# Performance work log

Hardware: AMD Instinct MI355X
Metric: run time of the kernel (lower is better)

The kernel has to match this reference:

```python
import jax, jax.numpy as jnp
import numpy as np
from jax import lax


def _conv(x, w, padding, groups=1):
    # NCHW / OIHW 2D conv, stride 1
    return lax.conv_general_dilated(
        x, w, window_strides=(1, 1), padding=padding,
        dimension_numbers=("NCHW", "OIHW", "NCHW"),
        feature_group_count=groups)


def setup_inputs() -> dict:
    key = jax.random.key(0)
    ks = jax.random.split(key, 5)
    B, C, H, W = 8, 192, 128, 128
    HEADS = 8
    rgb = jax.random.normal(ks[0], (B, C, H, W), dtype=jnp.float32)
    ir = jax.random.normal(ks[1], (B, C, H, W), dtype=jnp.float32)
    w_qkv = jax.random.normal(ks[2], (3 * C, C, 1, 1), dtype=jnp.float32) * 0.02
    w_dw = jax.random.normal(ks[3], (3 * C, 1, 3, 3), dtype=jnp.float32) * 0.02
    w_proj = jax.random.normal(ks[4], (C, C, 1, 1), dtype=jnp.float32) * 0.02
    temperature = jnp.ones((HEADS, 1, 1), dtype=jnp.float32)
    return {"rgb": rgb, "ir": ir, "w_qkv": w_qkv, "w_dw": w_dw,
            "w_proj": w_proj, "temperature": temperature}


def reference(rgb, ir, w_qkv, w_dw, w_proj, temperature):
    heads = temperature.shape[0]
    b, c, h, w = rgb.shape
    hd = c // heads  # per-head channel count

    def qkv(x):
        y = _conv(x, w_qkv, "VALID")                 # [b, 3c, h, w]
        y = _conv(y, w_dw, "SAME", groups=3 * c)      # depthwise 3x3
        q, k, v = jnp.split(y, 3, axis=1)
        rs = lambda t: t.reshape(b, heads, hd, h * w)  # b head c (h w)
        return rs(q), rs(k), rs(v)

    rq, rk, rv = qkv(rgb)
    iq, ik, iv = qkv(ir)

    # torch F.normalize(dim=-1): x / max(||x||_2, 1e-12)
    nrm = lambda t: t / jnp.maximum(jnp.linalg.norm(t, axis=-1, keepdims=True), 1e-12)
    rq, rk, iq, ik = nrm(rq), nrm(rk), nrm(iq), nrm(ik)

    # channel-wise (transposed) cross attention: [b,h,hd,hd] attn matrices
    attn_ir = jax.nn.softmax(jnp.einsum("bhcn,bhdn->bhcd", rq, ik) * temperature, axis=-1)
    attn_rgb = jax.nn.softmax(jnp.einsum("bhcn,bhdn->bhcd", iq, rk) * temperature, axis=-1)

    out_ir = jnp.einsum("bhcd,bhdn->bhcn", attn_ir, iv).reshape(b, c, h, w)
    out_rgb = jnp.einsum("bhcd,bhdn->bhcn", attn_rgb, rv).reshape(b, c, h, w)

    out_ir = _conv(out_ir, w_proj, "VALID")
    out_rgb = _conv(out_rgb, w_proj, "VALID")
    return out_rgb, out_ir
```

## Files before the change

kernel.cpp:

```cpp
#include <hip/hip_runtime.h>

#define N_PIX 16384
#define CC    192
#define C3    576
#define KK    192
#define HD    24
#define KS    64

typedef __attribute__((ext_vector_type(8))) short short8;
typedef __attribute__((ext_vector_type(4))) float f32x4;

__device__ __forceinline__ unsigned short f2bf(float x) {
    unsigned u = __float_as_uint(x);
    u += 0x7fff + ((u >> 16) & 1);
    return (unsigned short)(u >> 16);
}
__device__ __forceinline__ float bf2f(unsigned short s) {
    return __uint_as_float(((unsigned)s) << 16);
}
__device__ __forceinline__ int pack2(unsigned short lo, unsigned short hi) {
    return (int)(((unsigned)hi << 16) | (unsigned)lo);
}

__device__ __forceinline__ void g2l16(const unsigned short* g, unsigned short* l) {
    __builtin_amdgcn_global_load_lds(
        (const __attribute__((address_space(1))) void*)g,
        (__attribute__((address_space(3))) void*)l, 16, 0, 0);
}

__global__ __launch_bounds__(256) void cvt_f32_bf16(const float* __restrict__ src,
                                                    unsigned short* __restrict__ dst, int n4) {
    int i = blockIdx.x * 256 + threadIdx.x;
    if (i < n4) {
        float4 v = ((const float4*)src)[i];
        ushort4 o;
        o.x = f2bf(v.x); o.y = f2bf(v.y); o.z = f2bf(v.z); o.w = f2bf(v.w);
        ((ushort4*)dst)[i] = o;
    }
}

__global__ __launch_bounds__(256) void cvtT(const float* __restrict__ rgb,
                                            const float* __restrict__ ir,
                                            unsigned short* __restrict__ xT) {
    const int z  = blockIdx.y;
    const int n0 = blockIdx.x * 128;
    const float* x = ((z >= 8) ? ir : rgb) + (long)(z & 7) * CC * N_PIX;
    __shared__ unsigned short T[192][136];

    const int t = threadIdx.x;
#pragma unroll
    for (int i = 0; i < 24; i++) {
        int q = i * 256 + t;
        int k = q >> 5, nc = q & 31;
        float4 v = *(const float4*)(x + (long)k * N_PIX + n0 + nc * 4);
        ushort4 o;
        o.x = f2bf(v.x); o.y = f2bf(v.y); o.z = f2bf(v.z); o.w = f2bf(v.w);
        *(ushort4*)&T[k][nc * 4] = o;
    }
    __syncthreads();
    unsigned short* dst = xT + ((long)z * N_PIX + n0) * CC;
#pragma unroll
    for (int i = 0; i < 12; i++) {
        int c = i * 256 + t;
        int n = c / 24, kc = c - n * 24;
        unsigned short us[8];
#pragma unroll
        for (int j = 0; j < 8; j++) us[j] = T[kc * 8 + j][n];
        int4 pk = make_int4(pack2(us[0], us[1]), pack2(us[2], us[3]),
                            pack2(us[4], us[5]), pack2(us[6], us[7]));
        *(int4*)(dst + (long)n * CC + kc * 8) = pk;
    }
}

__global__ __launch_bounds__(512, 4) void qkv_mfma(const unsigned short* __restrict__ wbf,
                                                   const unsigned short* __restrict__ xT,
                                                   unsigned short* __restrict__ Ybf) {
    const int z  = blockIdx.z;
    const unsigned short* Bg = xT + (long)z * N_PIX * CC;
    unsigned short* y = Ybf + (long)z * C3 * N_PIX;
    const int m0 = blockIdx.y * 192, n0 = blockIdx.x * 128;

    __shared__ unsigned short As[2][192 * 64];
    __shared__ unsigned short Bs[2][128 * 64];

    const int tid  = threadIdx.x;
    const int wave = tid >> 6, lane = tid & 63;
    const int quad = lane >> 4, l15 = lane & 15;
    const int wr = wave >> 2, wc = wave & 3;

    f32x4 acc[6][2];
#pragma unroll
    for (int i = 0; i < 6; i++)
#pragma unroll
        for (int j = 0; j < 2; j++) acc[i][j] = (f32x4)0.f;

    auto stage = [&](int buf, int k0) {
#pragma unroll
        for (int s = 0; s < 3; s++) {
            int j = s * 8 + wave;
            int q = j * 64 + lane;
            int m = q >> 3, c = (q & 7) ^ (m & 7);
            g2l16(wbf + (long)(m0 + m) * KK + k0 + c * 8, &As[buf][j * 512]);
        }
#pragma unroll
        for (int s = 0; s < 2; s++) {
            int j = s * 8 + wave;
            int q = j * 64 + lane;
            int n = q >> 3, c = (q & 7) ^ (n & 7);
            g2l16(Bg + (long)(n0 + n) * CC + k0 + c * 8, &Bs[buf][j * 512]);
        }
    };

    stage(0, 0);
    __syncthreads();
    int cur = 0;
    for (int it = 0; it < 3; ++it) {
        if (it < 2) stage(cur ^ 1, (it + 1) * KS);
        const unsigned short* A  = As[cur];
        const unsigned short* Bl = Bs[cur];
#pragma unroll
        for (int kk = 0; kk < 2; kk++) {
            short8 a[6], b[2];
#pragma unroll
            for (int mi = 0; mi < 6; mi++) {
                int r = wr * 96 + mi * 16 + l15;
                int c = (kk * 4 + quad) ^ (r & 7);
                a[mi] = *(const short8*)&A[r * 64 + c * 8];
            }
#pragma unroll
            for (int ni = 0; ni < 2; ni++) {
                int n = wc * 32 + ni * 16 + l15;
                int c = (kk * 4 + quad) ^ (n & 7);
                b[ni] = *(const short8*)&Bl[n * 64 + c * 8];
            }
#pragma unroll
            for (int mi = 0; mi < 6; mi++)
#pragma unroll
                for (int ni = 0; ni < 2; ni++)
                    acc[mi][ni] = __builtin_amdgcn_mfma_f32_16x16x32_bf16(a[mi], b[ni], acc[mi][ni], 0, 0, 0);
        }
        __syncthreads();
        cur ^= 1;
    }

#pragma unroll
    for (int mi = 0; mi < 6; mi++)
#pragma unroll
        for (int ni = 0; ni < 2; ni++)
#pragma unroll
            for (int r = 0; r < 4; r++) {
                int row = m0 + wr * 96 + mi * 16 + quad * 4 + r;
                int col = n0 + wc * 32 + ni * 16 + l15;
                y[(long)row * N_PIX + col] = f2bf(acc[mi][ni][r]);
            }
}

__device__ __forceinline__ void mfma_gemm_old(const unsigned short* __restrict__ Abf,
                                              const unsigned short* __restrict__ Bsrc,
                                              float* __restrict__ Cdst,
                                              int m0, int n0) {
    __shared__ unsigned short As[192][44];
    __shared__ unsigned short Bs[128][44];

    const int tid  = threadIdx.x;
    const int wave = tid >> 6, lane = tid & 63;
    const int quad = lane >> 4, l15 = lane & 15;
    const int wr = wave >> 2, wc = wave & 3;

    f32x4 acc[6][2];
#pragma unroll
    for (int i = 0; i < 6; i++)
#pragma unroll
        for (int j = 0; j < 2; j++) acc[i][j] = (f32x4)0.f;

    const int kg = tid & 7;
    const int n2 = tid >> 3;

    for (int k0 = 0; k0 < KK; k0 += 32) {
        {
            int row = tid >> 2, kc = (tid & 3) * 8;
            *(int4*)&As[row][kc] = *(const int4*)(Abf + (long)(m0 + row) * KK + k0 + kc);
            if (tid < 256) {
                int ch = tid + 512;
                int row2 = ch >> 2, kc2 = (ch & 3) * 8;
                *(int4*)&As[row2][kc2] = *(const int4*)(Abf + (long)(m0 + row2) * KK + k0 + kc2);
            }
        }
        {
            ushort2 v[4];
#pragma unroll
            for (int j = 0; j < 4; j++)
                v[j] = *(const ushort2*)(Bsrc + (long)(k0 + kg * 4 + j) * N_PIX + n0 + n2 * 2);
#pragma unroll
            for (int i = 0; i < 2; i++) {
                unsigned short us[4];
#pragma unroll
                for (int j = 0; j < 4; j++) us[j] = i ? v[j].y : v[j].x;
                int2 pk = make_int2(pack2(us[0], us[1]), pack2(us[2], us[3]));
                *(int2*)&Bs[n2 * 2 + i][kg * 4] = pk;
            }
        }
        __syncthreads();

        short8 a[6], b[2];
#pragma unroll
        for (int mi = 0; mi < 6; mi++)
            a[mi] = *(const short8*)&As[wr * 96 + mi * 16 + l15][quad * 8];
#pragma unroll
        for (int ni = 0; ni < 2; ni++)
            b[ni] = *(const short8*)&Bs[wc * 32 + ni * 16 + l15][quad * 8];
#pragma unroll
        for (int mi = 0; mi < 6; mi++)
#pragma unroll
            for (int ni = 0; ni < 2; ni++)
                acc[mi][ni] = __builtin_amdgcn_mfma_f32_16x16x32_bf16(a[mi], b[ni], acc[mi][ni], 0, 0, 0);
        __syncthreads();
    }

#pragma unroll
    for (int mi = 0; mi < 6; mi++)
#pragma unroll
        for (int ni = 0; ni < 2; ni++)
#pragma unroll
            for (int r = 0; r < 4; r++) {
                int row = m0 + wr * 96 + mi * 16 + quad * 4 + r;
                int col = n0 + wc * 32 + ni * 16 + l15;
                Cdst[(long)row * N_PIX + col] = acc[mi][ni][r];
            }
}

__global__ __launch_bounds__(512, 4) void out_mfma(const unsigned short* __restrict__ weff,
                                                   const unsigned short* __restrict__ Zbf,
                                                   float* __restrict__ out) {
    const int z = blockIdx.z;
    const unsigned short* V = Zbf + ((long)z * C3 + 2 * CC) * N_PIX;
    float* C = out + (long)z * CC * N_PIX;
    mfma_gemm_old(weff + (long)z * CC * CC, V, C, 0, blockIdx.x * 128);
}

__global__ __launch_bounds__(256) void dwconv3x3(const unsigned short* __restrict__ Ybf,
                                                 const float* __restrict__ wdw,
                                                 unsigned short* __restrict__ Zbf) {
    const int z  = blockIdx.z;
    const int oc = blockIdx.y;
    const int idx = blockIdx.x * 256 + threadIdx.x;
    const int p0  = idx * 8;
    const int h   = p0 >> 7;
    const int w0  = p0 & 127;
    const int wq  = threadIdx.x & 15;
    const unsigned short* Yc = Ybf + ((long)z * C3 + oc) * N_PIX;

    float wk[9];
#pragma unroll
    for (int i = 0; i < 9; i++) wk[i] = wdw[oc * 9 + i];

    float f[3][8];
#pragma unroll
    for (int ry = 0; ry < 3; ry++) {
        const int hy = h + ry - 1;
        int4 raw = make_int4(0, 0, 0, 0);
        if (hy >= 0 && hy <= 127)
            raw = *(const int4*)(Yc + hy * 128 + w0);
        f[ry][0] = bf2f((unsigned short)(raw.x & 0xffff));
        f[ry][1] = bf2f((unsigned short)((unsigned)raw.x >> 16));
        f[ry][2] = bf2f((unsigned short)(raw.y & 0xffff));
        f[ry][3] = bf2f((unsigned short)((unsigned)raw.y >> 16));
        f[ry][4] = bf2f((unsigned short)(raw.z & 0xffff));
        f[ry][5] = bf2f((unsigned short)((unsigned)raw.z >> 16));
        f[ry][6] = bf2f((unsigned short)(raw.w & 0xffff));
        f[ry][7] = bf2f((unsigned short)((unsigned)raw.w >> 16));
    }

    float acc[8];
#pragma unroll
    for (int j = 0; j < 8; j++) acc[j] = 0.f;

#pragma unroll
    for (int ry = 0; ry < 3; ry++) {
        float l = __shfl_up(f[ry][7], 1);
        float r = __shfl_down(f[ry][0], 1);
        if (wq == 0)  l = 0.f;
        if (wq == 15) r = 0.f;
        const float wl = wk[ry * 3 + 0], wc = wk[ry * 3 + 1], wr = wk[ry * 3 + 2];
        acc[0] = fmaf(wl, l, acc[0]);
#pragma unroll
        for (int j = 1; j < 8; j++) acc[j] = fmaf(wl, f[ry][j - 1], acc[j]);
#pragma unroll
        for (int j = 0; j < 8; j++) acc[j] = fmaf(wc, f[ry][j], acc[j]);
#pragma unroll
        for (int j = 0; j < 7; j++) acc[j] = fmaf(wr, f[ry][j + 1], acc[j]);
        acc[7] = fmaf(wr, r, acc[7]);
    }

    ushort4 o[2];
    unsigned short* po = (unsigned short*)o;
#pragma unroll
    for (int j = 0; j < 8; j++) po[j] = f2bf(acc[j]);
    *(int4*)(Zbf + ((long)z * C3 + oc) * N_PIX + p0) = *(const int4*)o;
}

__global__ __launch_bounds__(64) void gram_partial(const unsigned short* __restrict__ Zbf,
                                                   float* __restrict__ gpart) {
    const int split = blockIdx.x;
    const int bh    = blockIdx.y;
    const int which = blockIdx.z;
    const int b = bh >> 3, head = bh & 7;
    const int zq = (which == 0) ? b : 8 + b;
    const int zk = (which == 0) ? 8 + b : b;
    const unsigned short* Q  = Zbf + ((long)zq * C3 + head * HD) * N_PIX;
    const unsigned short* Kr = Zbf + ((long)zk * C3 + CC + head * HD) * N_PIX;

    __shared__ float Qc[24][132];
    __shared__ float Kc[24][132];

    const int t = threadIdx.x;
    const int ci = t >> 3, di = t & 7;
    const int c0 = ci * 3, d0 = di * 3;

    float acc[3][3];
#pragma unroll
    for (int i = 0; i < 3; i++)
#pragma unroll
        for (int j = 0; j < 3; j++) acc[i][j] = 0.f;
    float ss = 0.f;

    const int n0base = split * 2048;
    for (int nc = 0; nc < 2048; nc += 128) {
        const long n0 = n0base + nc;
        const unsigned short* src = nullptr;
        float* dstrow = nullptr;
        if (t < 24)               { src = Q  + (long)t * N_PIX + n0;        dstrow = Qc[t]; }
        else if (t >= 32 && t < 56) { src = Kr + (long)(t - 32) * N_PIX + n0; dstrow = Kc[t - 32]; }
        if (src) {
#pragma unroll 4
            for (int i = 0; i < 16; i++) {
                int4 raw = *(const int4*)(src + i * 8);
                float f[8];
                f[0] = bf2f((unsigned short)(raw.x & 0xffff)); f[1] = bf2f((unsigned short)((unsigned)raw.x >> 16));
                f[2] = bf2f((unsigned short)(raw.y & 0xffff)); f[3] = bf2f((unsigned short)((unsigned)raw.y >> 16));
                f[4] = bf2f((unsigned short)(raw.z & 0xffff)); f[5] = bf2f((unsigned short)((unsigned)raw.z >> 16));
                f[6] = bf2f((unsigned short)(raw.w & 0xffff)); f[7] = bf2f((unsigned short)((unsigned)raw.w >> 16));
                *(float4*)&dstrow[i * 8]     = make_float4(f[0], f[1], f[2], f[3]);
                *(float4*)&dstrow[i * 8 + 4] = make_float4(f[4], f[5], f[6], f[7]);
#pragma unroll
                for (int q = 0; q < 8; q++) ss = fmaf(f[q], f[q], ss);
            }
        }
        __syncthreads();
#pragma unroll 4
        for (int kk = 0; kk < 128; kk += 4) {
            float4 qv[3], kv[3];
#pragma unroll
            for (int i = 0; i < 3; i++) qv[i] = *(const float4*)&Qc[c0 + i][kk];
#pragma unroll
            for (int j = 0; j < 3; j++) kv[j] = *(const float4*)&Kc[d0 + j][kk];
#pragma unroll
            for (int i = 0; i < 3; i++)
#pragma unroll
                for (int j = 0; j < 3; j++)
                    acc[i][j] += qv[i].x * kv[j].x + qv[i].y * kv[j].y +
                                 qv[i].z * kv[j].z + qv[i].w * kv[j].w;
        }
        __syncthreads();
    }

    const int g = (which * 64 + bh) * 8 + split;
    float* gp = gpart + (long)g * 624;
#pragma unroll
    for (int i = 0; i < 3; i++)
#pragma unroll
        for (int j = 0; j < 3; j++)
            gp[(c0 + i) * 24 + (d0 + j)] = acc[i][j];
    if (t < 24) gp[576 + t] = ss;
    else if (t >= 32 && t < 56) gp[600 + (t - 32)] = ss;
}

__global__ __launch_bounds__(256) void gram_reduce_softmax(const float* __restrict__ gpart,
                                                           const float* __restrict__ temperature,
                                                           float* __restrict__ P) {
    const int g = blockIdx.x;
    const int head = g & 7;
    __shared__ float Gs[576];
    __shared__ float qs[24], ks[24], invq[24], invk[24];

    const int t = threadIdx.x;
    for (int e = t; e < 624; e += 256) {
        float s = 0.f;
        for (int sp = 0; sp < 8; sp++) s += gpart[(long)(g * 8 + sp) * 624 + e];
        if (e < 576) Gs[e] = s;
        else if (e < 600) qs[e - 576] = s;
        else ks[e - 600] = s;
    }
    __syncthreads();
    if (t < 24) {
        invq[t] = 1.f / fmaxf(sqrtf(qs[t]), 1e-12f);
        invk[t] = 1.f / fmaxf(sqrtf(ks[t]), 1e-12f);
    }
    __syncthreads();
    if (t < 24) {
        const float temp = temperature[head];
        float row[24];
        float m = -1e30f;
#pragma unroll
        for (int d = 0; d < 24; d++) {
            row[d] = Gs[t * 24 + d] * invq[t] * invk[d] * temp;
            m = fmaxf(m, row[d]);
        }
        float ssum = 0.f;
#pragma unroll
        for (int d = 0; d < 24; d++) {
            row[d] = expf(row[d] - m);
            ssum += row[d];
        }
        const float inv = 1.f / ssum;
#pragma unroll
        for (int d = 0; d < 24; d++)
            P[(long)g * 576 + t * 24 + d] = row[d] * inv;
    }
}

__global__ __launch_bounds__(256) void build_weff(const float* __restrict__ wproj,
                                                  const float* __restrict__ P,
                                                  unsigned short* __restrict__ weff) {
    const int o = blockIdx.z, b = blockIdx.y;
    const int e = blockIdx.x * 256 + threadIdx.x;
    const int co = e / 192, col = e % 192;
    const int head = col / 24, d = col % 24;
    const int which = 1 - o;
    const float* Pp = P + (long)(which * 64 + b * 8 + head) * 576;
    const float* wp = wproj + co * 192 + head * 24;
    float acc = 0.f;
#pragma unroll
    for (int hc = 0; hc < 24; hc++)
        acc = fmaf(wp[hc], Pp[hc * 24 + d], acc);
    weff[((long)(o * 8 + b) * 192 + co) * 192 + col] = f2bf(acc);
}

extern "C" void kernel_launch(void* const* d_in, const int* in_sizes, int n_in,
                              void* d_out, int out_size, void* d_ws, size_t ws_size,
                              hipStream_t stream) {
    (void)in_sizes; (void)n_in; (void)out_size; (void)ws_size;
    const float* rgb    = (const float*)d_in[0];
    const float* ir     = (const float*)d_in[1];
    const float* w_qkv  = (const float*)d_in[2];
    const float* w_dw   = (const float*)d_in[3];
    const float* w_proj = (const float*)d_in[4];
    const float* temp   = (const float*)d_in[5];
    float* out = (float*)d_out;

    char* wsb = (char*)d_ws;
    unsigned short* Y_bf    = (unsigned short*)(wsb);
    unsigned short* Z_bf    = (unsigned short*)(wsb + 301989888L);
    unsigned short* xT_bf   = Z_bf;
    unsigned short* w_bf    = (unsigned short*)(wsb + 603979776L);
    unsigned short* weff_bf = (unsigned short*)(wsb + 604200960L);
    float*          gpart   = (float*)(wsb + 605380608L);
    float*          P       = (float*)(wsb + 607936512L);

    cvt_f32_bf16<<<108, 256, 0, stream>>>(w_qkv, w_bf, 27648);
    cvtT<<<dim3(128, 16), 256, 0, stream>>>(rgb, ir, xT_bf);
    qkv_mfma<<<dim3(128, 3, 16), 512, 0, stream>>>(w_bf, xT_bf, Y_bf);
    dwconv3x3<<<dim3(8, 576, 16), 256, 0, stream>>>(Y_bf, w_dw, Z_bf);
    gram_partial<<<dim3(8, 64, 2), 64, 0, stream>>>(Z_bf, gpart);
    gram_reduce_softmax<<<128, 256, 0, stream>>>(gpart, temp, P);
    build_weff<<<dim3(144, 8, 2), 256, 0, stream>>>(w_proj, P, weff_bf);
    out_mfma<<<dim3(128, 1, 16), 512, 0, stream>>>(weff_bf, Z_bf, out);
}
```

Before: 799.4 us.

## Compute Q·K Gram matrices with MFMA and fuse L2 norms into dwconv

Replaces the scalar fp32 per-head Gram kernel with a bf16 MFMA kernel. Each block computes the full 192x192 Q·K^T product for one batch/direction over a 512-pixel slice and keeps only the diagonal 24x24 head blocks. The squared-norm accumulation moves into the depthwise conv epilogue through wave reductions and atomics, and the softmax kernel now reads those norms and sums 32 split partials. This computes 8x more products than needed (off-diagonal blocks are discarded), adds atomics and a zeroing launch, and reuses the Y buffer region for the partials.

```diff
diff --git a/kernel.cpp b/kernel.cpp
--- a/kernel.cpp
+++ b/kernel.cpp
@@ -5,7 +5,7 @@
 #define C3    576
 #define KK    192
 #define HD    24
-#define KS    64
+#define GSPLIT 32
 
 typedef __attribute__((ext_vector_type(8))) short short8;
 typedef __attribute__((ext_vector_type(4))) float f32x4;
@@ -39,6 +39,11 @@
     }
 }
 
+__global__ __launch_bounds__(256) void zero_f32(float* __restrict__ p, int n) {
+    int i = blockIdx.x * 256 + threadIdx.x;
+    if (i < n) p[i] = 0.f;
+}
+
 __global__ __launch_bounds__(256) void cvtT(const float* __restrict__ rgb,
                                             const float* __restrict__ ir,
                                             unsigned short* __restrict__ xT) {
@@ -115,7 +120,7 @@
     __syncthreads();
     int cur = 0;
     for (int it = 0; it < 3; ++it) {
-        if (it < 2) stage(cur ^ 1, (it + 1) * KS);
+        if (it < 2) stage(cur ^ 1, (it + 1) * 64);
         const unsigned short* A  = As[cur];
         const unsigned short* Bl = Bs[cur];
 #pragma unroll
@@ -152,6 +157,90 @@
                 int row = m0 + wr * 96 + mi * 16 + quad * 4 + r;
                 int col = n0 + wc * 32 + ni * 16 + l15;
                 y[(long)row * N_PIX + col] = f2bf(acc[mi][ni][r]);
+            }
+}
+
+__global__ __launch_bounds__(512, 2) void gram_mfma(const unsigned short* __restrict__ Zbf,
+                                                    float* __restrict__ gpart) {
+    const int ks = blockIdx.x;
+    const int zp = blockIdx.y;
+    const int which = zp >> 3, b = zp & 7;
+    const int zq = which ? 8 + b : b;
+    const int zk = which ? b : 8 + b;
+    const unsigned short* Qg = Zbf + (long)zq * C3 * N_PIX;
+    const unsigned short* Kg = Zbf + ((long)zk * C3 + CC) * N_PIX;
+
+    __shared__ unsigned short Qs[2][192 * 64];
+    __shared__ unsigned short Ks[2][192 * 64];
+
+    const int tid  = threadIdx.x;
+    const int wave = tid >> 6, lane = tid & 63;
+    const int quad = lane >> 4, l15 = lane & 15;
+    const int wr = wave >> 1, wc = wave & 1;
+
+    f32x4 acc[3][6];
+#pragma unroll
+    for (int i = 0; i < 3; i++)
+#pragma unroll
+        for (int j = 0; j < 6; j++) acc[i][j] = (f32x4)0.f;
+
+    const int base = ks * 512;
+
+    auto stage = [&](int buf, int k0) {
+#pragma unroll
+        for (int s = 0; s < 3; s++) {
+            int j = s * 8 + wave;
+            int q = j * 64 + lane;
+            int m = q >> 3, c = (q & 7) ^ (m & 7);
+            g2l16(Qg + (long)m * N_PIX + k0 + c * 8, &Qs[buf][j * 512]);
+            g2l16(Kg + (long)m * N_PIX + k0 + c * 8, &Ks[buf][j * 512]);
+        }
+    };
+
+    stage(0, base);
+    __syncthreads();
+    int cur = 0;
+    for (int it = 0; it < 8; ++it) {
+        if (it < 7) stage(cur ^ 1, base + (it + 1) * 64);
+        const unsigned short* Q = Qs[cur];
+        const unsigned short* Kl = Ks[cur];
+#pragma unroll
+        for (int kk = 0; kk < 2; kk++) {
+            short8 a[3], bf[6];
+#pragma unroll
+            for (int mi = 0; mi < 3; mi++) {
+                int r = wr * 48 + mi * 16 + l15;
+                int c = (kk * 4 + quad) ^ (r & 7);
+                a[mi] = *(const short8*)&Q[r * 64 + c * 8];
+            }
+#pragma unroll
+            for (int ni = 0; ni < 6; ni++) {
+                int n = wc * 96 + ni * 16 + l15;
+                int c = (kk * 4 + quad) ^ (n & 7);
+                bf[ni] = *(const short8*)&Kl[n * 64 + c * 8];
+            }
+#pragma unroll
+            for (int mi = 0; mi < 3; mi++)
+#pragma unroll
+                for (int ni = 0; ni < 6; ni++)
+                    acc[mi][ni] = __builtin_amdgcn_mfma_f32_16x16x32_bf16(a[mi], bf[ni], acc[mi][ni], 0, 0, 0);
+        }
+        __syncthreads();
+        cur ^= 1;
+    }
+
+#pragma unroll
+    for (int mi = 0; mi < 3; mi++)
+#pragma unroll
+        for (int ni = 0; ni < 6; ni++)
+#pragma unroll
+            for (int r = 0; r < 4; r++) {
+                int row = wr * 48 + mi * 16 + quad * 4 + r;
+                int col = wc * 96 + ni * 16 + l15;
+                int hr = row / 24, hc = col / 24;
+                if (hr == hc)
+                    gpart[(((long)zp * GSPLIT + ks) * 8 + hr) * 576 +
+                          (row - hr * 24) * 24 + (col - hc * 24)] = acc[mi][ni][r];
             }
 }
 
@@ -240,7 +329,8 @@
 
 __global__ __launch_bounds__(256) void dwconv3x3(const unsigned short* __restrict__ Ybf,
                                                  const float* __restrict__ wdw,
-                                                 unsigned short* __restrict__ Zbf) {
+                                                 unsigned short* __restrict__ Zbf,
+                                                 float* __restrict__ norm) {
     const int z  = blockIdx.z;
     const int oc = blockIdx.y;
     const int idx = blockIdx.x * 256 + threadIdx.x;
@@ -297,105 +387,45 @@
 #pragma unroll
     for (int j = 0; j < 8; j++) po[j] = f2bf(acc[j]);
     *(int4*)(Zbf + ((long)z * C3 + oc) * N_PIX + p0) = *(const int4*)o;
-}
-
-__global__ __launch_bounds__(64) void gram_partial(const unsigned short* __restrict__ Zbf,
-                                                   float* __restrict__ gpart) {
-    const int split = blockIdx.x;
-    const int bh    = blockIdx.y;
-    const int which = blockIdx.z;
-    const int b = bh >> 3, head = bh & 7;
-    const int zq = (which == 0) ? b : 8 + b;
-    const int zk = (which == 0) ? 8 + b : b;
-    const unsigned short* Q  = Zbf + ((long)zq * C3 + head * HD) * N_PIX;
-    const unsigned short* Kr = Zbf + ((long)zk * C3 + CC + head * HD) * N_PIX;
-
-    __shared__ float Qc[24][132];
-    __shared__ float Kc[24][132];
-
-    const int t = threadIdx.x;
-    const int ci = t >> 3, di = t & 7;
-    const int c0 = ci * 3, d0 = di * 3;
-
-    float acc[3][3];
-#pragma unroll
-    for (int i = 0; i < 3; i++)
-#pragma unroll
-        for (int j = 0; j < 3; j++) acc[i][j] = 0.f;
-    float ss = 0.f;
-
-    const int n0base = split * 2048;
-    for (int nc = 0; nc < 2048; nc += 128) {
-        const long n0 = n0base + nc;
-        const unsigned short* src = nullptr;
-        float* dstrow = nullptr;
-        if (t < 24)               { src = Q  + (long)t * N_PIX + n0;        dstrow = Qc[t]; }
-        else if (t >= 32 && t < 56) { src = Kr + (long)(t - 32) * N_PIX + n0; dstrow = Kc[t - 32]; }
-        if (src) {
-#pragma unroll 4
-            for (int i = 0; i < 16; i++) {
-                int4 raw = *(const int4*)(src + i * 8);
-                float f[8];
-                f[0] = bf2f((unsigned short)(raw.x & 0xffff)); f[1] = bf2f((unsigned short)((unsigned)raw.x >> 16));
-                f[2] = bf2f((unsigned short)(raw.y & 0xffff)); f[3] = bf2f((unsigned short)((unsigned)raw.y >> 16));
-                f[4] = bf2f((unsigned short)(raw.z & 0xffff)); f[5] = bf2f((unsigned short)((unsigned)raw.z >> 16));
-                f[6] = bf2f((unsigned short)(raw.w & 0xffff)); f[7] = bf2f((unsigned short)((unsigned)raw.w >> 16));
-                *(float4*)&dstrow[i * 8]     = make_float4(f[0], f[1], f[2], f[3]);
-                *(float4*)&dstrow[i * 8 + 4] = make_float4(f[4], f[5], f[6], f[7]);
-#pragma unroll
-                for (int q = 0; q < 8; q++) ss = fmaf(f[q], f[q], ss);
-            }
-        }
-        __syncthreads();
-#pragma unroll 4
-        for (int kk = 0; kk < 128; kk += 4) {
-            float4 qv[3], kv[3];
-#pragma unroll
-            for (int i = 0; i < 3; i++) qv[i] = *(const float4*)&Qc[c0 + i][kk];
-#pragma unroll
-            for (int j = 0; j < 3; j++) kv[j] = *(const float4*)&Kc[d0 + j][kk];
-#pragma unroll
-            for (int i = 0; i < 3; i++)
-#pragma unroll
-                for (int j = 0; j < 3; j++)
-                    acc[i][j] += qv[i].x * kv[j].x + qv[i].y * kv[j].y +
-                                 qv[i].z * kv[j].z + qv[i].w * kv[j].w;
-        }
-        __syncthreads();
-    }
-
-    const int g = (which * 64 + bh) * 8 + split;
-    float* gp = gpart + (long)g * 624;
-#pragma unroll
-    for (int i = 0; i < 3; i++)
-#pragma unroll
-        for (int j = 0; j < 3; j++)
-            gp[(c0 + i) * 24 + (d0 + j)] = acc[i][j];
-    if (t < 24) gp[576 + t] = ss;
-    else if (t >= 32 && t < 56) gp[600 + (t - 32)] = ss;
+
+    if (oc < 2 * CC) {
+        float ss = 0.f;
+#pragma unroll
+        for (int j = 0; j < 8; j++) {
+            float v = bf2f(po[j]);
+            ss = fmaf(v, v, ss);
+        }
+#pragma unroll
+        for (int off = 32; off > 0; off >>= 1)
+            ss += __shfl_down(ss, off);
+        if ((threadIdx.x & 63) == 0)
+            atomicAdd(&norm[z * (2 * CC) + oc], ss);
+    }
 }
 
 __global__ __launch_bounds__(256) void gram_reduce_softmax(const float* __restrict__ gpart,
+                                                           const float* __restrict__ norm,
                                                            const float* __restrict__ temperature,
                                                            float* __restrict__ P) {
     const int g = blockIdx.x;
-    const int head = g & 7;
+    const int which = g >> 6, b = (g >> 3) & 7, head = g & 7;
+    const int zp = which * 8 + b;
+    const int zq = which ? 8 + b : b;
+    const int zk = which ? b : 8 + b;
     __shared__ float Gs[576];
-    __shared__ float qs[24], ks[24], invq[24], invk[24];
+    __shared__ float invq[24], invk[24];
 
     const int t = threadIdx.x;
-    for (int e = t; e < 624; e += 256) {
+    for (int e = t; e < 576; e += 256) {
         float s = 0.f;
-        for (int sp = 0; sp < 8; sp++) s += gpart[(long)(g * 8 + sp) * 624 + e];
-        if (e < 576) Gs[e] = s;
-        else if (e < 600) qs[e - 576] = s;
-        else ks[e - 600] = s;
-    }
-    __syncthreads();
-    if (t < 24) {
-        invq[t] = 1.f / fmaxf(sqrtf(qs[t]), 1e-12f);
-        invk[t] = 1.f / fmaxf(sqrtf(ks[t]), 1e-12f);
-    }
+        for (int sp = 0; sp < GSPLIT; sp++)
+            s += gpart[(((long)zp * GSPLIT + sp) * 8 + head) * 576 + e];
+        Gs[e] = s;
+    }
+    if (t < 24)
+        invq[t] = 1.f / fmaxf(sqrtf(norm[zq * (2 * CC) + head * HD + t]), 1e-12f);
+    else if (t >= 32 && t < 56)
+        invk[t - 32] = 1.f / fmaxf(sqrtf(norm[zk * (2 * CC) + CC + head * HD + (t - 32)]), 1e-12f);
     __syncthreads();
     if (t < 24) {
         const float temp = temperature[head];
@@ -452,17 +482,19 @@
     unsigned short* Y_bf    = (unsigned short*)(wsb);
     unsigned short* Z_bf    = (unsigned short*)(wsb + 301989888L);
     unsigned short* xT_bf   = Z_bf;
+    float*          gpart   = (float*)(wsb);
     unsigned short* w_bf    = (unsigned short*)(wsb + 603979776L);
     unsigned short* weff_bf = (unsigned short*)(wsb + 604200960L);
-    float*          gpart   = (float*)(wsb + 605380608L);
+    float*          norm    = (float*)(wsb + 605380608L);
     float*          P       = (float*)(wsb + 607936512L);
 
     cvt_f32_bf16<<<108, 256, 0, stream>>>(w_qkv, w_bf, 27648);
     cvtT<<<dim3(128, 16), 256, 0, stream>>>(rgb, ir, xT_bf);
+    zero_f32<<<24, 256, 0, stream>>>(norm, 16 * 2 * CC);
     qkv_mfma<<<dim3(128, 3, 16), 512, 0, stream>>>(w_bf, xT_bf, Y_bf);
-    dwconv3x3<<<dim3(8, 576, 16), 256, 0, stream>>>(Y_bf, w_dw, Z_bf);
-    gram_partial<<<dim3(8, 64, 2), 64, 0, stream>>>(Z_bf, gpart);
-    gram_reduce_softmax<<<128, 256, 0, stream>>>(gpart, temp, P);
+    dwconv3x3<<<dim3(8, 576, 16), 256, 0, stream>>>(Y_bf, w_dw, Z_bf, norm);
+    gram_mfma<<<dim3(GSPLIT, 16), 512, 0, stream>>>(Z_bf, gpart);
+    gram_reduce_softmax<<<128, 256, 0, stream>>>(gpart, norm, temp, P);
     build_weff<<<dim3(144, 8, 2), 256, 0, stream>>>(w_proj, P, weff_bf);
     out_mfma<<<dim3(128, 1, 16), 512, 0, stream>>>(weff_bf, Z_bf, out);
 }
```

Result: faster. 753.7 us (-5.7%).
